# Performance work log

Measured on AMD Instinct MI355X. Metric: run time of the kernel, lower is better.

## Reference

```python
import jax, jax.numpy as jnp
import numpy as np

B, S, E, H = 2, 2048, 1024, 16
Dh = E // H
LN_EPS = 1e-5


def setup_inputs() -> dict:
    key = jax.random.key(0)
    ks = jax.random.split(key, 12)
    std = 1.0 / np.sqrt(E)
    inp = {
        "query": jax.random.normal(ks[0], (B, S, E), jnp.float32),
        "key":   jax.random.normal(ks[1], (B, S, E), jnp.float32),
        "value": jax.random.normal(ks[2], (B, S, E), jnp.float32),
        # True = masked. Causal mask so every row keeps >=1 valid entry.
        "mask": jnp.broadcast_to(jnp.triu(jnp.ones((S, S), bool), k=1), (B, S, S)),
        # per-head QKV projections, stacked: weight [H, Dh, E] (torch Linear layout), bias [H, Dh]
        "Wq_w": jax.random.uniform(ks[3], (H, Dh, E), jnp.float32, -std, std),
        "Wq_b": jax.random.uniform(ks[4], (H, Dh), jnp.float32, -std, std),
        "Wk_w": jax.random.uniform(ks[5], (H, Dh, E), jnp.float32, -std, std),
        "Wk_b": jax.random.uniform(ks[6], (H, Dh), jnp.float32, -std, std),
        "Wv_w": jax.random.uniform(ks[7], (H, Dh, E), jnp.float32, -std, std),
        "Wv_b": jax.random.uniform(ks[8], (H, Dh), jnp.float32, -std, std),
        # output projection [E, E] (torch layout: out = x @ W.T + b)
        "out_w": jax.random.uniform(ks[9], (E, E), jnp.float32, -std, std),
        "out_b": jax.random.uniform(ks[10], (E,), jnp.float32, -std, std),
        "ln_g": jnp.ones((E,), jnp.float32),
        "ln_b": jnp.zeros((E,), jnp.float32),
    }
    return inp


def reference(query, key, value, mask, Wq_w, Wq_b, Wk_w, Wk_b, Wv_w, Wv_b, out_w, out_b, ln_g, ln_b):
    # per-head projections (batched over heads): [B,S,E] x [H,Dh,E] -> [B,H,S,Dh]
    q = jnp.einsum('bse,hde->bhsd', query, Wq_w) + Wq_b[None, :, None, :]
    k = jnp.einsum('bse,hde->bhsd', key,   Wk_w) + Wk_b[None, :, None, :]
    v = jnp.einsum('bse,hde->bhsd', value, Wv_w) + Wv_b[None, :, None, :]
    scale = 1.0 / np.sqrt(Dh).astype(np.float32)
    scores = jnp.einsum('bhsd,bhtd->bhst', q, k) * scale  # [B,H,S,S]
    scores = jnp.where(mask[:, None, :, :], -jnp.inf, scores)
    probs = jax.nn.softmax(scores, axis=-1)  # dropout p=0 (eval)
    ctx = jnp.einsum('bhst,bhtd->bhsd', probs, v)  # [B,H,S,Dh]
    att = ctx.transpose(0, 2, 1, 3).reshape(query.shape[0], query.shape[1], -1)  # concat heads [B,S,E]
    proj = att @ out_w.T + out_b  # dropout p=0
    x = query + proj  # residual
    mu = jnp.mean(x, axis=-1, keepdims=True)
    var = jnp.mean(jnp.square(x - mu), axis=-1, keepdims=True)
    return (x - mu) * jax.lax.rsqrt(var + LN_EPS) * ln_g + ln_b
```

## Files before the change

### kernel.cpp

```cpp
#include <hip/hip_runtime.h>
#include <stdint.h>

#define B_ 2
#define S_ 2048
#define E_ 1024
#define H_ 16
#define DH 64
#define M_TOT (B_*S_)

typedef short s16x8 __attribute__((ext_vector_type(8)));
typedef float f32x4 __attribute__((ext_vector_type(4)));
typedef unsigned int u32;
typedef unsigned short u16;

union V8 { uint4 u; s16x8 v; };

__device__ __forceinline__ u32 fbits(float f){ union{float f;u32 i;}x; x.f=f; return x.i; }
__device__ __forceinline__ u32 prround(float f){ return fbits(f)+0x8000u; }
__device__ __forceinline__ u16 f2bf(float f){ return (u16)(prround(f)>>16); }
__device__ __forceinline__ u32 permpack(u32 hi,u32 lo){ return __builtin_amdgcn_perm(hi,lo,0x07060302u); }
__device__ __forceinline__ uint4 pack8r(const float4 a, const float4 b){
    uint4 p;
    p.x = permpack(prround(a.y),prround(a.x));
    p.y = permpack(prround(a.w),prround(a.z));
    p.z = permpack(prround(b.y),prround(b.x));
    p.w = permpack(prround(b.w),prround(b.z));
    return p;
}
__device__ __forceinline__ float exp2_fast(float x){ float r; asm("v_exp_f32 %0, %1":"=v"(r):"v"(x)); return r; }

typedef const __attribute__((address_space(1))) u32* gas_t;
typedef __attribute__((address_space(3))) u32* las_t;
#define GLDS16(gp, lp) __builtin_amdgcn_global_load_lds((gas_t)(gp), (las_t)(lp), 16, 0, 0)

#define MFMA16(a,b,c) __builtin_amdgcn_mfma_f32_16x16x32_bf16((a),(b),(c),0,0,0)

__global__ __launch_bounds__(256) void cvtw(
    const float* __restrict__ w0, const float* __restrict__ w1, const float* __restrict__ w2,
    u16* __restrict__ dst, int n4)
{
    const int z = blockIdx.y;
    const float* s = (z==0)?w0:(z==1)?w1:w2;
    u16* d = dst + (size_t)z*E_*E_;
    int i = blockIdx.x*256 + threadIdx.x;
    const int stride = gridDim.x*256;
    for (; i<n4; i+=stride){
        float4 v = ((const float4*)s)[i];
        uint2 p;
        p.x = permpack(prround(v.y),prround(v.x));
        p.y = permpack(prround(v.w),prround(v.z));
        ((uint2*)d)[i] = p;
    }
}
__global__ __launch_bounds__(256) void cvt1(
    const float* __restrict__ s, u16* __restrict__ d, int n4)
{
    int i = blockIdx.x*256 + threadIdx.x;
    const int stride = gridDim.x*256;
    for (; i<n4; i+=stride){
        float4 v = ((const float4*)s)[i];
        uint2 p;
        p.x = permpack(prround(v.y),prround(v.x));
        p.y = permpack(prround(v.w),prround(v.z));
        ((uint2*)d)[i] = p;
    }
}

__global__ __launch_bounds__(256,3) void qkv128(
    const float* __restrict__ xq, const float* __restrict__ xk, const float* __restrict__ xv,
    const u16* __restrict__ Wb,
    const float* __restrict__ bq, const float* __restrict__ bk, const float* __restrict__ bv,
    u16* __restrict__ oq, u16* __restrict__ ok_, u16* __restrict__ ovt)
{
    const int bid = blockIdx.x;
    const int c = bid & 7;
    const int tdec = bid >> 3;
    const int n = tdec & 7;
    const int g = ((tdec >> 3) << 3) + c;
    const int m = g & 31, z = g >> 5;

    const float* X = (z==0)?xq:(z==1)?xk:xv;
    const u16* W = Wb + (size_t)z*E_*E_;
    const float* bia = (z==0)?bq:(z==1)?bk:bv;
    const float scale = (z==0)? 0.125f*1.44269504f : 1.0f;

    __shared__ __align__(16) u16 As[3][128*32];
    __shared__ __align__(16) u16 Bs[3][128*32];

    const int tid = threadIdx.x;
    const int wid = tid>>6, lane = tid&63;
    const int lrow = lane&15, quad = lane>>4;
    const int mb = m*128, nb = n*128;
    const int wm = (wid>>1)*64, wn = (wid&1)*64;
    const int srow = lane>>2, skq = lane&3;
    const int arow = wid*32 + (lane>>1);
    const int akh  = lane&1;
    const int ag0  = akh*2;
    const int asw  = arow&3;

    f32x4 acc[4][4] = {};
    const float* Xb = X + (size_t)mb*E_;
    const u16*  Wn = W + (size_t)nb*E_;
    const float* Xrow = Xb + (size_t)arow*E_ + akh*16;

    float4 arA0, arA1, arA2, arA3;
    float4 arB0, arB1, arB2, arB3;

    auto stageB = [&](u16* Bd, int kt){
        const int k0 = kt*32;
#pragma unroll
        for (int i=0;i<2;i++){
            const int rb = wid*32 + i*16;
            GLDS16(Wn + (size_t)(rb+srow)*E_ + k0 + ((skq^(srow&3))<<3), Bd + rb*32);
        }
    };

#define QKV_ISSUEA(KT, AR) do {                                   \
        const float* xp_ = Xrow + ((KT)<<5);                      \
        AR##0 = *(const float4*)(xp_    );                        \
        AR##1 = *(const float4*)(xp_ + 4);                        \
        AR##2 = *(const float4*)(xp_ + 8);                        \
        AR##3 = *(const float4*)(xp_ +12);                        \
    } while(0)

#define QKV_WRITEA(AD, AR) do {                                   \
        const uint4 w0_ = pack8r(AR##0, AR##1);                   \
        const uint4 w1_ = pack8r(AR##2, AR##3);                   \
        *(uint4*)&(AD)[arow*32 + (((ag0  )^asw)<<3)] = w0_;       \
        *(uint4*)&(AD)[arow*32 + (((ag0+1)^asw)<<3)] = w1_;       \
    } while(0)

#define QKV_ITER(KT, TC, ARC, ARN) do {                                       \
        const int ts_ = ((KT)+2 < 32) ? (KT)+2 : 31;                          \
        const int tw_ = ((TC)+1==3)?0:(TC)+1;                                 \
        const int tn_ = (tw_+1==3)?0:tw_+1;                                   \
        const u16* Ad_ = As[TC];                                              \
        const u16* Bd_ = Bs[TC];                                              \
        asm volatile("s_waitcnt vmcnt(6) lgkmcnt(0)" ::: "memory");           \
        __builtin_amdgcn_s_barrier();                                         \
        __builtin_amdgcn_sched_barrier(0);                                    \
        const int fq_ = (quad^(lrow&3))<<3;                                   \
        s16x8 a0 = *(const s16x8*)&Ad_[(wm+ 0+lrow)*32 + fq_];                \
        s16x8 a1 = *(const s16x8*)&Ad_[(wm+16+lrow)*32 + fq_];                \
        s16x8 a2 = *(const s16x8*)&Ad_[(wm+32+lrow)*32 + fq_];                \
        s16x8 a3 = *(const s16x8*)&Ad_[(wm+48+lrow)*32 + fq_];                \
        s16x8 b0 = *(const s16x8*)&Bd_[(wn+ 0+lrow)*32 + fq_];                \
        s16x8 b1 = *(const s16x8*)&Bd_[(wn+16+lrow)*32 + fq_];                \
        s16x8 b2 = *(const s16x8*)&Bd_[(wn+32+lrow)*32 + fq_];                \
        s16x8 b3 = *(const s16x8*)&Bd_[(wn+48+lrow)*32 + fq_];                \
        __builtin_amdgcn_sched_barrier(0);                                    \
        QKV_ISSUEA(ts_, ARN);                                                 \
        __builtin_amdgcn_sched_barrier(0);                                    \
        stageB(Bs[tn_], ts_);                                                 \
        __builtin_amdgcn_sched_barrier(0);                                    \
        __builtin_amdgcn_s_setprio(1);                                        \
        acc[0][0] = MFMA16(a0, b0, acc[0][0]);                                \
        acc[0][1] = MFMA16(a0, b1, acc[0][1]);                                \
        acc[0][2] = MFMA16(a0, b2, acc[0][2]);                                \
        acc[0][3] = MFMA16(a0, b3, acc[0][3]);                                \
        acc[1][0] = MFMA16(a1, b0, acc[1][0]);                                \
        acc[1][1] = MFMA16(a1, b1, acc[1][1]);                                \
        acc[1][2] = MFMA16(a1, b2, acc[1][2]);                                \
        acc[1][3] = MFMA16(a1, b3, acc[1][3]);                                \
        __builtin_amdgcn_s_setprio(0);                                        \
        QKV_WRITEA(As[tw_], ARC);                                             \
        __builtin_amdgcn_s_setprio(1);                                        \
        acc[2][0] = MFMA16(a2, b0, acc[2][0]);                                \
        acc[2][1] = MFMA16(a2, b1, acc[2][1]);                                \
        acc[2][2] = MFMA16(a2, b2, acc[2][2]);                                \
        acc[2][3] = MFMA16(a2, b3, acc[2][3]);                                \
        acc[3][0] = MFMA16(a3, b0, acc[3][0]);                                \
        acc[3][1] = MFMA16(a3, b1, acc[3][1]);                                \
        acc[3][2] = MFMA16(a3, b2, acc[3][2]);                                \
        acc[3][3] = MFMA16(a3, b3, acc[3][3]);                                \
        __builtin_amdgcn_s_setprio(0);                                        \
    } while(0)

    QKV_ISSUEA(0, arA);
    stageB(Bs[0], 0);
    QKV_WRITEA(As[0], arA);
    QKV_ISSUEA(1, arA);
    stageB(Bs[1], 1);

    int tc = 0;
#pragma unroll 1
    for (int k2=0; k2<16; ++k2){
        const int kt0 = k2*2;
        QKV_ITER(kt0,   tc, arA, arB);
        tc = (tc+1==3)?0:tc+1;
        QKV_ITER(kt0+1, tc, arB, arA);
        tc = (tc+1==3)?0:tc+1;
    }
    asm volatile("s_waitcnt vmcnt(0) lgkmcnt(0)" ::: "memory");

#undef QKV_ITER
#undef QKV_WRITEA
#undef QKV_ISSUEA

    if (z < 2){
        u16* O = (z==0)?oq:ok_;
#pragma unroll
        for (int ci=0;ci<4;ci++){
            const int nn = nb+wn+ci*16+lrow;
            const float bval = bia[nn];
            const int h = nn>>6, d = nn&63;
#pragma unroll
            for (int mi=0;mi<4;mi++){
#pragma unroll
                for (int r=0;r<4;r++){
                    const int mm = mb+wm+mi*16+quad*4+r;
                    const int bb = mm>>11, s = mm&(S_-1);
                    O[(((size_t)(bb*H_+h))*S_+s)*DH + d] = f2bf((acc[mi][ci][r]+bval)*scale);
                }
            }
        }
    } else {
#pragma unroll
        for (int ci=0;ci<4;ci++){
            const int nn = nb+wn+ci*16+lrow;
            const float bval = bia[nn];
            const int h = nn>>6, d = nn&63;
#pragma unroll
            for (int mi=0;mi<4;mi++){
                const int m0 = mb+wm+mi*16+quad*4;
                const int bb = m0>>11, s0 = m0&(S_-1);
                uint2 pk;
                pk.x = permpack(prround(acc[mi][ci][1]+bval), prround(acc[mi][ci][0]+bval));
                pk.y = permpack(prround(acc[mi][ci][3]+bval), prround(acc[mi][ci][2]+bval));
                *(uint2*)&ovt[(((size_t)(bb*H_+h))*DH + d)*S_ + s0] = pk;
            }
        }
    }
}

__global__ __launch_bounds__(256) void attn(
    const u16* __restrict__ q_ws, const u16* __restrict__ k_ws,
    const u16* __restrict__ vt_ws, u16* __restrict__ att)
{
    const int bid = blockIdx.x;
    const int c8 = bid & 7;
    const int t = bid >> 3;
    const int p = t & 15;
    const int bh = ((t >> 4) << 3) + c8;
    const int b = bh>>4, h = bh&15;

    const u16* Qb = q_ws + (size_t)bh*S_*DH;
    const u16* Kb = k_ws + (size_t)bh*S_*DH;
    const u16* VT = vt_ws + (size_t)bh*DH*S_;

    __shared__ __align__(16) u16 Ks0[64*64];
    __shared__ __align__(16) u16 Ks1[64*64];
    __shared__ __align__(16) u16 Vt0[64*64];
    __shared__ __align__(16) u16 Vt1[64*64];
    __shared__ __align__(16) u16 Ps[4][16*64];

    const int tid = threadIdx.x;
    const int wid = tid>>6, lane = tid&63;
    const int lrow = lane&15, quad = lane>>4;
    u16* Pw = Ps[wid];

    const int srw = lane>>3;
    const int scs = lane&7;
    const int sgc = scs ^ srw;

    auto stageKV = [&](u16* Kd, u16* Vd, int t0){
#pragma unroll
        for (int g2=0; g2<2; g2++){
            const int rg = wid*16 + g2*8 + srw;
            GLDS16(Kb + (size_t)(t0+rg)*DH + (sgc<<3), Kd + (wid*16+g2*8)*64);
            GLDS16(VT + (size_t)rg*S_ + t0 + (sgc<<3), Vd + (wid*16+g2*8)*64);
        }
    };

    for (int ph=0; ph<2; ph++){
        const int qi = ph ? (31-p) : p;
        const int qb = qi<<6;

        s16x8 qf[2];
#pragma unroll
        for (int ch=0;ch<2;ch++)
            qf[ch] = *(const s16x8*)&Qb[(size_t)(qb+wid*16+lrow)*DH + ch*32 + quad*8];

        f32x4 o[4] = {};
        float l_lane = 0.f;
        const int qglob = qb + wid*16 + lrow;
        const int ntile = qi + 1;

        auto computeTile = [&](const u16* Kd, const u16* Vd, int t0, bool diag){
            f32x4 st[4] = {};
#pragma unroll
            for (int tt=0;tt<4;tt++){
                const int tr = tt*16+lrow;
#pragma unroll
                for (int ch=0;ch<2;ch++){
                    const int slot = (ch*4+quad) ^ (lrow&7);
                    const s16x8 kf = *(const s16x8*)&Kd[tr*64 + slot*8];
                    st[tt] = __builtin_amdgcn_mfma_f32_16x16x32_bf16(kf, qf[ch], st[tt],0,0,0);
                }
            }
            if (diag){
#pragma unroll
                for (int tt=0;tt<4;tt++){
                    const int tg = t0 + tt*16 + quad*4;
#pragma unroll
                    for (int r=0;r<4;r++)
                        if (tg + r > qglob) st[tt][r] = -1e30f;
                }
            }
#pragma unroll
            for (int tt=0;tt<4;tt++){
                const float p0 = exp2_fast(st[tt][0]);
                const float p1 = exp2_fast(st[tt][1]);
                const float p2 = exp2_fast(st[tt][2]);
                const float p3 = exp2_fast(st[tt][3]);
                l_lane += (p0+p1)+(p2+p3);
                const int tc = tt*2 + (quad>>1);
                const int ts = tc ^ (lrow&7);
                const int a0 = lrow*64 + ts*8 + (quad&1)*4;
                *(u32*)&Pw[a0]   = permpack(prround(p1),prround(p0));
                *(u32*)&Pw[a0+2] = permpack(prround(p3),prround(p2));
            }
            s16x8 pb[2];
#pragma unroll
            for (int ch=0;ch<2;ch++){
                const int slot = (ch*4+quad) ^ (lrow&7);
                pb[ch] = *(const s16x8*)&Pw[lrow*64 + slot*8];
            }
#pragma unroll
            for (int cc=0;cc<4;cc++){
                const int vr = cc*16+lrow;
#pragma unroll
                for (int ch=0;ch<2;ch++){
                    const int slot = (ch*4+quad) ^ (lrow&7);
                    const s16x8 vf = *(const s16x8*)&Vd[vr*64 + slot*8];
                    o[cc] = __builtin_amdgcn_mfma_f32_16x16x32_bf16(vf, pb[ch], o[cc],0,0,0);
                }
            }
        };

        __syncthreads();
        stageKV(Ks0, Vt0, 0);
        for (int ti=0; ; ti+=2){
            __syncthreads();
            if (ti+1 < ntile) stageKV(Ks1, Vt1, (ti+1)<<6);
            computeTile(Ks0, Vt0, ti<<6, ti==ntile-1);
            if (ti+1 >= ntile) break;
            __syncthreads();
            if (ti+2 < ntile) stageKV(Ks0, Vt0, (ti+2)<<6);
            computeTile(Ks1, Vt1, (ti+1)<<6, ti+1==ntile-1);
            if (ti+2 >= ntile) break;
        }

        float s = l_lane;
        s += __shfl_xor(s, 16, 64);
        s += __shfl_xor(s, 32, 64);
        const float rl = 1.0f/s;

#pragma unroll
        for (int cc=0;cc<4;cc++){
            uint2 pk;
            pk.x = permpack(prround(o[cc][1]*rl), prround(o[cc][0]*rl));
            pk.y = permpack(prround(o[cc][3]*rl), prround(o[cc][2]*rl));
            *(uint2*)&att[(size_t)(b*S_ + qglob)*E_ + h*DH + cc*16 + quad*4] = pk;
        }
    }
}

__global__ __launch_bounds__(256) void oproj128(
    const u16* __restrict__ A, const u16* __restrict__ W, const float* __restrict__ bias,
    const float* __restrict__ resid, float* __restrict__ out)
{
    const int bid = blockIdx.x;
    const int c = bid & 7;
    const int tdec = bid >> 3;
    const int n = tdec & 15;
    const int m = ((tdec >> 4) << 3) + c;

    __shared__ __align__(16) u16 As[3][128*32];
    __shared__ __align__(16) u16 Bs[3][64*32];

    const int tid = threadIdx.x;
    const int wid = tid>>6, lane = tid&63;
    const int lrow = lane&15, quad = lane>>4;
    const int mb = m*128, nb = n*64;
    const int srow = lane>>2, skq = lane&3;

    f32x4 acc[2][4] = {};
    const u16* Ab = A + (size_t)mb*E_;
    const u16* Wn = W + (size_t)nb*E_;

    auto stage = [&](u16* Ad, u16* Bd, int kt){
        const int k0 = kt*32;
        const int kc = (skq^(srow&3))<<3;
#pragma unroll
        for (int i=0;i<2;i++){
            const int rb = wid*32 + i*16;
            GLDS16(Ab + (size_t)(rb+srow)*E_ + k0 + kc, Ad + rb*32);
        }
        GLDS16(Wn + (size_t)(wid*16+srow)*E_ + k0 + kc, Bd + (wid*16)*32);
    };

    stage(As[0], Bs[0], 0);
    stage(As[1], Bs[1], 1);

    int tc = 0, tn = 2;
    for (int kt=0; kt<32; ++kt){
        const int ts = (kt+2 < 32) ? kt+2 : 31;
        asm volatile("s_waitcnt vmcnt(3) lgkmcnt(0)" ::: "memory");
        __builtin_amdgcn_s_barrier();
        __builtin_amdgcn_sched_barrier(0);

        const u16* Ad = As[tc];
        const u16* Bd = Bs[tc];
        const int sw = lrow&3;
        s16x8 a0 = *(const s16x8*)&Ad[(wid*32+ 0+lrow)*32 + ((quad^sw)<<3)];
        s16x8 a1 = *(const s16x8*)&Ad[(wid*32+16+lrow)*32 + ((quad^sw)<<3)];
        s16x8 b0 = *(const s16x8*)&Bd[( 0+lrow)*32 + ((quad^sw)<<3)];
        s16x8 b1 = *(const s16x8*)&Bd[(16+lrow)*32 + ((quad^sw)<<3)];
        s16x8 b2 = *(const s16x8*)&Bd[(32+lrow)*32 + ((quad^sw)<<3)];
        s16x8 b3 = *(const s16x8*)&Bd[(48+lrow)*32 + ((quad^sw)<<3)];
        stage(As[tn], Bs[tn], ts);
        __builtin_amdgcn_s_setprio(1);
        acc[0][0] = MFMA16(a0, b0, acc[0][0]);
        acc[0][1] = MFMA16(a0, b1, acc[0][1]);
        acc[0][2] = MFMA16(a0, b2, acc[0][2]);
        acc[0][3] = MFMA16(a0, b3, acc[0][3]);
        acc[1][0] = MFMA16(a1, b0, acc[1][0]);
        acc[1][1] = MFMA16(a1, b1, acc[1][1]);
        acc[1][2] = MFMA16(a1, b2, acc[1][2]);
        acc[1][3] = MFMA16(a1, b3, acc[1][3]);
        __builtin_amdgcn_s_setprio(0);
        tc = (tc+1==3)?0:tc+1;
        tn = (tn+1==3)?0:tn+1;
    }
    asm volatile("s_waitcnt vmcnt(0)" ::: "memory");

#pragma unroll
    for (int ci=0;ci<4;ci++){
        const int nn = nb+ci*16+lrow;
        const float bval = bias[nn];
#pragma unroll
        for (int mi=0;mi<2;mi++){
#pragma unroll
            for (int r=0;r<4;r++){
                const int mm = mb+wid*32+mi*16+quad*4+r;
                out[(size_t)mm*E_+nn] = acc[mi][ci][r] + bval + resid[(size_t)mm*E_+nn];
            }
        }
    }
}

__global__ __launch_bounds__(256) void ln_k(
    const float* __restrict__ xin, const float* __restrict__ lg,
    const float* __restrict__ lb, float* __restrict__ out)
{
    const int row = blockIdx.x;
    const int tid = threadIdx.x;
    const int wid = tid>>6, lane = tid&63;
    const float* xr = xin + (size_t)row*E_;

    float x[4];
    float s = 0.f;
#pragma unroll
    for (int i=0;i<4;i++){ const int e = i*256+tid; x[i] = xr[e]; s += x[i]; }
    __shared__ float red[8];
#pragma unroll
    for (int off=32; off>0; off>>=1) s += __shfl_xor(s, off, 64);
    if (lane==0) red[wid] = s;
    __syncthreads();
    const float mu = (red[0]+red[1]+red[2]+red[3]) * (1.f/E_);

    float v = 0.f;
#pragma unroll
    for (int i=0;i<4;i++){ const float d = x[i]-mu; v += d*d; }
#pragma unroll
    for (int off=32; off>0; off>>=1) v += __shfl_xor(v, off, 64);
    if (lane==0) red[wid+4] = v;
    __syncthreads();
    const float var = (red[4]+red[5]+red[6]+red[7]) * (1.f/E_);
    const float rs = rsqrtf(var + 1e-5f);

#pragma unroll
    for (int i=0;i<4;i++){
        const int e = i*256+tid;
        out[(size_t)row*E_+e] = (x[i]-mu)*rs*lg[e] + lb[e];
    }
}

extern "C" void kernel_launch(void* const* d_in, const int* in_sizes, int n_in,
                              void* d_out, int out_size, void* d_ws, size_t ws_size,
                              hipStream_t stream) {
    const float* q_in = (const float*)d_in[0];
    const float* k_in = (const float*)d_in[1];
    const float* v_in = (const float*)d_in[2];
    const float* wq = (const float*)d_in[4];
    const float* bq = (const float*)d_in[5];
    const float* wk = (const float*)d_in[6];
    const float* bk = (const float*)d_in[7];
    const float* wv = (const float*)d_in[8];
    const float* bv = (const float*)d_in[9];
    const float* ow = (const float*)d_in[10];
    const float* ob = (const float*)d_in[11];
    const float* lg = (const float*)d_in[12];
    const float* lb = (const float*)d_in[13];
    float* out = (float*)d_out;

    char* ws = (char*)d_ws;
    const size_t MB = (size_t)1<<20;
    u16* q_ws  = (u16*)(ws);
    u16* k_ws  = (u16*)(ws +  8*MB);
    u16* vt_ws = (u16*)(ws + 16*MB);
    u16* att   = (u16*)(ws + 24*MB);
    u16* Wbf   = (u16*)(ws + 24*MB);
    u16* owbf  = (u16*)(ws + 16*MB);
    float* proj = (float*)ws;

    cvtw<<<dim3(512,3), 256, 0, stream>>>(wq, wk, wv, Wbf, (E_*E_)/4);
    qkv128<<<dim3(768), 256, 0, stream>>>(
        q_in, k_in, v_in, Wbf, bq, bk, bv, q_ws, k_ws, vt_ws);
    attn<<<dim3(512), 256, 0, stream>>>(q_ws, k_ws, vt_ws, att);
    cvt1<<<dim3(1024), 256, 0, stream>>>(ow, owbf, (E_*E_)/4);
    oproj128<<<dim3(512), 256, 0, stream>>>(att, owbf, ob, q_in, proj);
    ln_k<<<dim3(M_TOT), 256, 0, stream>>>(proj, lg, lb, out);
}
```

Baseline: 249.2 us.

## Split attention to one query tile per block and narrow output-projection tiles

```diff
diff --git a/kernel.cpp b/kernel.cpp
--- a/kernel.cpp
+++ b/kernel.cpp
@@ -233,15 +233,15 @@
     }
 }
 
-__global__ __launch_bounds__(256) void attn(
+__global__ __launch_bounds__(256,4) void attn(
     const u16* __restrict__ q_ws, const u16* __restrict__ k_ws,
     const u16* __restrict__ vt_ws, u16* __restrict__ att)
 {
     const int bid = blockIdx.x;
     const int c8 = bid & 7;
-    const int t = bid >> 3;
-    const int p = t & 15;
-    const int bh = ((t >> 4) << 3) + c8;
+    const int k = bid >> 3;
+    const int bh = ((k >> 5) << 3) + c8;
+    const int qi = (13*(k & 31) + 7*(k >> 5)) & 31;
     const int b = bh>>4, h = bh&15;
 
     const u16* Qb = q_ws + (size_t)bh*S_*DH;
@@ -272,124 +272,121 @@
         }
     };
 
-    for (int ph=0; ph<2; ph++){
-        const int qi = ph ? (31-p) : p;
-        const int qb = qi<<6;
-
-        s16x8 qf[2];
-#pragma unroll
-        for (int ch=0;ch<2;ch++)
-            qf[ch] = *(const s16x8*)&Qb[(size_t)(qb+wid*16+lrow)*DH + ch*32 + quad*8];
-
-        f32x4 o[4] = {};
-        float l_lane = 0.f;
-        const int qglob = qb + wid*16 + lrow;
-        const int ntile = qi + 1;
-
-        auto computeTile = [&](const u16* Kd, const u16* Vd, int t0, bool diag){
-            f32x4 st[4] = {};
-#pragma unroll
-            for (int tt=0;tt<4;tt++){
-                const int tr = tt*16+lrow;
-#pragma unroll
-                for (int ch=0;ch<2;ch++){
-                    const int slot = (ch*4+quad) ^ (lrow&7);
-                    const s16x8 kf = *(const s16x8*)&Kd[tr*64 + slot*8];
-                    st[tt] = __builtin_amdgcn_mfma_f32_16x16x32_bf16(kf, qf[ch], st[tt],0,0,0);
-                }
-            }
-            if (diag){
-#pragma unroll
-                for (int tt=0;tt<4;tt++){
-                    const int tg = t0 + tt*16 + quad*4;
-#pragma unroll
-                    for (int r=0;r<4;r++)
-                        if (tg + r > qglob) st[tt][r] = -1e30f;
-                }
-            }
-#pragma unroll
-            for (int tt=0;tt<4;tt++){
-                const float p0 = exp2_fast(st[tt][0]);
-                const float p1 = exp2_fast(st[tt][1]);
-                const float p2 = exp2_fast(st[tt][2]);
-                const float p3 = exp2_fast(st[tt][3]);
-                l_lane += (p0+p1)+(p2+p3);
-                const int tc = tt*2 + (quad>>1);
-                const int ts = tc ^ (lrow&7);
-                const int a0 = lrow*64 + ts*8 + (quad&1)*4;
-                *(u32*)&Pw[a0]   = permpack(prround(p1),prround(p0));
-                *(u32*)&Pw[a0+2] = permpack(prround(p3),prround(p2));
-            }
-            s16x8 pb[2];
+    const int qb = qi<<6;
+
+    s16x8 qf[2];
+#pragma unroll
+    for (int ch=0;ch<2;ch++)
+        qf[ch] = *(const s16x8*)&Qb[(size_t)(qb+wid*16+lrow)*DH + ch*32 + quad*8];
+
+    f32x4 o[4] = {};
+    float l_lane = 0.f;
+    const int qglob = qb + wid*16 + lrow;
+    const int ntile = qi + 1;
+
+    auto computeTile = [&](const u16* Kd, const u16* Vd, int t0, bool diag){
+        f32x4 st[4] = {};
+#pragma unroll
+        for (int tt=0;tt<4;tt++){
+            const int tr = tt*16+lrow;
 #pragma unroll
             for (int ch=0;ch<2;ch++){
                 const int slot = (ch*4+quad) ^ (lrow&7);
-                pb[ch] = *(const s16x8*)&Pw[lrow*64 + slot*8];
+                const s16x8 kf = *(const s16x8*)&Kd[tr*64 + slot*8];
+                st[tt] = __builtin_amdgcn_mfma_f32_16x16x32_bf16(kf, qf[ch], st[tt],0,0,0);
             }
-#pragma unroll
-            for (int cc=0;cc<4;cc++){
-                const int vr = cc*16+lrow;
-#pragma unroll
-                for (int ch=0;ch<2;ch++){
-                    const int slot = (ch*4+quad) ^ (lrow&7);
-                    const s16x8 vf = *(const s16x8*)&Vd[vr*64 + slot*8];
-                    o[cc] = __builtin_amdgcn_mfma_f32_16x16x32_bf16(vf, pb[ch], o[cc],0,0,0);
-                }
+        }
+        if (diag){
+#pragma unroll
+            for (int tt=0;tt<4;tt++){
+                const int tg = t0 + tt*16 + quad*4;
+#pragma unroll
+                for (int r=0;r<4;r++)
+                    if (tg + r > qglob) st[tt][r] = -1e30f;
             }
-        };
-
+        }
+#pragma unroll
+        for (int tt=0;tt<4;tt++){
+            const float p0 = exp2_fast(st[tt][0]);
+            const float p1 = exp2_fast(st[tt][1]);
+            const float p2 = exp2_fast(st[tt][2]);
+            const float p3 = exp2_fast(st[tt][3]);
+            l_lane += (p0+p1)+(p2+p3);
+            const int tc = tt*2 + (quad>>1);
+            const int ts = tc ^ (lrow&7);
+            const int a0 = lrow*64 + ts*8 + (quad&1)*4;
+            *(u32*)&Pw[a0]   = permpack(prround(p1),prround(p0));
+            *(u32*)&Pw[a0+2] = permpack(prround(p3),prround(p2));
+        }
+        s16x8 pb[2];
+#pragma unroll
+        for (int ch=0;ch<2;ch++){
+            const int slot = (ch*4+quad) ^ (lrow&7);
+            pb[ch] = *(const s16x8*)&Pw[lrow*64 + slot*8];
+        }
+#pragma unroll
+        for (int cc=0;cc<4;cc++){
+            const int vr = cc*16+lrow;
+#pragma unroll
+            for (int ch=0;ch<2;ch++){
+                const int slot = (ch*4+quad) ^ (lrow&7);
+                const s16x8 vf = *(const s16x8*)&Vd[vr*64 + slot*8];
+                o[cc] = __builtin_amdgcn_mfma_f32_16x16x32_bf16(vf, pb[ch], o[cc],0,0,0);
+            }
+        }
+    };
+
+    stageKV(Ks0, Vt0, 0);
+    for (int ti=0; ; ti+=2){
         __syncthreads();
-        stageKV(Ks0, Vt0, 0);
-        for (int ti=0; ; ti+=2){
-            __syncthreads();
-            if (ti+1 < ntile) stageKV(Ks1, Vt1, (ti+1)<<6);
-            computeTile(Ks0, Vt0, ti<<6, ti==ntile-1);
-            if (ti+1 >= ntile) break;
-            __syncthreads();
-            if (ti+2 < ntile) stageKV(Ks0, Vt0, (ti+2)<<6);
-            computeTile(Ks1, Vt1, (ti+1)<<6, ti+1==ntile-1);
-            if (ti+2 >= ntile) break;
-        }
-
-        float s = l_lane;
-        s += __shfl_xor(s, 16, 64);
-        s += __shfl_xor(s, 32, 64);
-        const float rl = 1.0f/s;
-
-#pragma unroll
-        for (int cc=0;cc<4;cc++){
-            uint2 pk;
-            pk.x = permpack(prround(o[cc][1]*rl), prround(o[cc][0]*rl));
-            pk.y = permpack(prround(o[cc][3]*rl), prround(o[cc][2]*rl));
-            *(uint2*)&att[(size_t)(b*S_ + qglob)*E_ + h*DH + cc*16 + quad*4] = pk;
-        }
-    }
-}
-
-__global__ __launch_bounds__(256) void oproj128(
+        if (ti+1 < ntile) stageKV(Ks1, Vt1, (ti+1)<<6);
+        computeTile(Ks0, Vt0, ti<<6, ti==ntile-1);
+        if (ti+1 >= ntile) break;
+        __syncthreads();
+        if (ti+2 < ntile) stageKV(Ks0, Vt0, (ti+2)<<6);
+        computeTile(Ks1, Vt1, (ti+1)<<6, ti+1==ntile-1);
+        if (ti+2 >= ntile) break;
+    }
+
+    float s = l_lane;
+    s += __shfl_xor(s, 16, 64);
+    s += __shfl_xor(s, 32, 64);
+    const float rl = 1.0f/s;
+
+#pragma unroll
+    for (int cc=0;cc<4;cc++){
+        uint2 pk;
+        pk.x = permpack(prround(o[cc][1]*rl), prround(o[cc][0]*rl));
+        pk.y = permpack(prround(o[cc][3]*rl), prround(o[cc][2]*rl));
+        *(uint2*)&att[(size_t)(b*S_ + qglob)*E_ + h*DH + cc*16 + quad*4] = pk;
+    }
+}
+
+__global__ __launch_bounds__(256,4) void oproj128(
     const u16* __restrict__ A, const u16* __restrict__ W, const float* __restrict__ bias,
     const float* __restrict__ resid, float* __restrict__ out)
 {
     const int bid = blockIdx.x;
     const int c = bid & 7;
-    const int tdec = bid >> 3;
-    const int n = tdec & 15;
-    const int m = ((tdec >> 4) << 3) + c;
+    const int kdec = bid >> 3;
+    const int n = kdec & 31;
+    const int m = ((kdec >> 5) << 3) + c;
 
     __shared__ __align__(16) u16 As[3][128*32];
-    __shared__ __align__(16) u16 Bs[3][64*32];
+    __shared__ __align__(16) u16 Bs[3][32*64];
 
     const int tid = threadIdx.x;
     const int wid = tid>>6, lane = tid&63;
     const int lrow = lane&15, quad = lane>>4;
-    const int mb = m*128, nb = n*64;
+    const int mb = m*128, nb = n*32;
     const int srow = lane>>2, skq = lane&3;
-
-    f32x4 acc[2][4] = {};
+    const int brow = lane>>3, bkq = lane&7;
+
+    f32x4 acc[2][2] = {};
     const u16* Ab = A + (size_t)mb*E_;
     const u16* Wn = W + (size_t)nb*E_;
 
-    auto stage = [&](u16* Ad, u16* Bd, int kt){
+    auto stageA = [&](u16* Ad, int kt){
         const int k0 = kt*32;
         const int kc = (skq^(srow&3))<<3;
 #pragma unroll
@@ -397,46 +394,50 @@
             const int rb = wid*32 + i*16;
             GLDS16(Ab + (size_t)(rb+srow)*E_ + k0 + kc, Ad + rb*32);
         }
-        GLDS16(Wn + (size_t)(wid*16+srow)*E_ + k0 + kc, Bd + (wid*16)*32);
     };
-
-    stage(As[0], Bs[0], 0);
-    stage(As[1], Bs[1], 1);
-
-    int tc = 0, tn = 2;
+    auto stageB = [&](u16* Bd, int pr){
+        GLDS16(Wn + (size_t)(wid*8+brow)*E_ + pr*64 + ((bkq^brow)<<3), Bd + (wid*8)*64);
+    };
+
+    stageA(As[0], 0); stageB(Bs[0], 0);
+    stageA(As[1], 1); stageB(Bs[1], 1);
+
+    int tc = 0;
+#pragma unroll 1
     for (int kt=0; kt<32; ++kt){
-        const int ts = (kt+2 < 32) ? kt+2 : 31;
+        const int pr = kt>>1, q = kt&1;
         asm volatile("s_waitcnt vmcnt(3) lgkmcnt(0)" ::: "memory");
         __builtin_amdgcn_s_barrier();
         __builtin_amdgcn_sched_barrier(0);
 
         const u16* Ad = As[tc];
-        const u16* Bd = Bs[tc];
-        const int sw = lrow&3;
-        s16x8 a0 = *(const s16x8*)&Ad[(wid*32+ 0+lrow)*32 + ((quad^sw)<<3)];
-        s16x8 a1 = *(const s16x8*)&Ad[(wid*32+16+lrow)*32 + ((quad^sw)<<3)];
-        s16x8 b0 = *(const s16x8*)&Bd[( 0+lrow)*32 + ((quad^sw)<<3)];
-        s16x8 b1 = *(const s16x8*)&Bd[(16+lrow)*32 + ((quad^sw)<<3)];
-        s16x8 b2 = *(const s16x8*)&Bd[(32+lrow)*32 + ((quad^sw)<<3)];
-        s16x8 b3 = *(const s16x8*)&Bd[(48+lrow)*32 + ((quad^sw)<<3)];
-        stage(As[tn], Bs[tn], ts);
+        const u16* Bd = Bs[pr%3];
+        const int fqA = (quad^(lrow&3))<<3;
+        s16x8 a0 = *(const s16x8*)&Ad[(wid*32+ 0+lrow)*32 + fqA];
+        s16x8 a1 = *(const s16x8*)&Ad[(wid*32+16+lrow)*32 + fqA];
+        const int sB = ((q*4+quad) ^ (lrow&7))<<3;
+        s16x8 b0 = *(const s16x8*)&Bd[( 0+lrow)*64 + sB];
+        s16x8 b1 = *(const s16x8*)&Bd[(16+lrow)*64 + sB];
+        __builtin_amdgcn_sched_barrier(0);
+        const int ta = (kt+2 < 32) ? kt+2 : 31;
+        stageA(As[(kt+2)%3], ta);
+        if (q==0){
+            const int pb = (pr+2 < 16) ? pr+2 : 15;
+            stageB(Bs[(pr+2)%3], pb);
+        }
+        __builtin_amdgcn_sched_barrier(0);
         __builtin_amdgcn_s_setprio(1);
         acc[0][0] = MFMA16(a0, b0, acc[0][0]);
         acc[0][1] = MFMA16(a0, b1, acc[0][1]);
-        acc[0][2] = MFMA16(a0, b2, acc[0][2]);
-        acc[0][3] = MFMA16(a0, b3, acc[0][3]);
         acc[1][0] = MFMA16(a1, b0, acc[1][0]);
         acc[1][1] = MFMA16(a1, b1, acc[1][1]);
-        acc[1][2] = MFMA16(a1, b2, acc[1][2]);
-        acc[1][3] = MFMA16(a1, b3, acc[1][3]);
         __builtin_amdgcn_s_setprio(0);
         tc = (tc+1==3)?0:tc+1;
-        tn = (tn+1==3)?0:tn+1;
     }
     asm volatile("s_waitcnt vmcnt(0)" ::: "memory");
 
 #pragma unroll
-    for (int ci=0;ci<4;ci++){
+    for (int ci=0;ci<2;ci++){
         const int nn = nb+ci*16+lrow;
         const float bval = bias[nn];
 #pragma unroll
@@ -518,8 +519,8 @@
     cvtw<<<dim3(512,3), 256, 0, stream>>>(wq, wk, wv, Wbf, (E_*E_)/4);
     qkv128<<<dim3(768), 256, 0, stream>>>(
         q_in, k_in, v_in, Wbf, bq, bk, bv, q_ws, k_ws, vt_ws);
-    attn<<<dim3(512), 256, 0, stream>>>(q_ws, k_ws, vt_ws, att);
+    attn<<<dim3(1024), 256, 0, stream>>>(q_ws, k_ws, vt_ws, att);
     cvt1<<<dim3(1024), 256, 0, stream>>>(ow, owbf, (E_*E_)/4);
-    oproj128<<<dim3(512), 256, 0, stream>>>(att, owbf, ob, q_in, proj);
+    oproj128<<<dim3(1024), 256, 0, stream>>>(att, owbf, ob, q_in, proj);
     ln_k<<<dim3(M_TOT), 256, 0, stream>>>(proj, lg, lb, out);
 }
```

Result: slower. 260.7 us (+4.6%).
